# Kernel optimization log

Hardware: AMD Instinct MI355X
Metric: run time of the kernel (lower is better)

The kernel has to match this reference:

```python
import jax, jax.numpy as jnp
import numpy as np

NC = 80
REG = 16          # DFL bins per coordinate
CONF_THRES = 0.25
IOU_THRES = 0.45
MAX_DET = 300
TOPK = 1000       # fixed-size pre-NMS candidate pool (stand-in for max_nms=30000 with A=8400)
MAX_WH = 7680.0   # class offset for class-aware NMS
LEVELS = [(80, 80, 8.0), (40, 40, 16.0), (20, 20, 32.0)]  # (h, w, stride) for imgsz=640


def _make_anchors():
    """make_anchors: grid-cell centers (+0.5 offset) and per-anchor strides."""
    pts, strs = [], []
    for h, w, s in LEVELS:
        sx = jnp.arange(w, dtype=jnp.float32) + 0.5
        sy = jnp.arange(h, dtype=jnp.float32) + 0.5
        gy, gx = jnp.meshgrid(sy, sx, indexing='ij')
        pts.append(jnp.stack([gx, gy], -1).reshape(-1, 2))
        strs.append(jnp.full((h * w,), s, dtype=jnp.float32))
    return jnp.concatenate(pts).T, jnp.concatenate(strs)  # [2, A], [A]


def _box_iou(b):  # b: [K, 4] xyxy -> [K, K] pairwise IoU
    area = (b[:, 2] - b[:, 0]) * (b[:, 3] - b[:, 1])
    lt = jnp.maximum(b[:, None, :2], b[None, :, :2])
    rb = jnp.minimum(b[:, None, 2:], b[None, :, 2:])
    wh = jnp.clip(rb - lt, 0.0)
    inter = wh[..., 0] * wh[..., 1]
    return inter / (area[:, None] + area[None, :] - inter + 1e-7)


def _nms_keep(iou, valid):
    """Greedy NMS over score-sorted candidates: keep[i] iff valid and no earlier kept box overlaps > thr."""
    K = iou.shape[0]
    idx = jnp.arange(K)
    def body(keep, i):
        sup = jnp.any((iou[i] > IOU_THRES) & keep & (idx < i))
        return keep.at[i].set(valid[i] & jnp.logical_not(sup)), None
    keep, _ = jax.lax.scan(body, jnp.zeros(K, dtype=bool), idx)
    return keep


def _forward(preds, dfl_w):
    B, C, A = preds.shape
    # DFL decode: softmax over 16 bins, expectation with arange(16) weights (the 1x1 conv)
    box_logits = preds[:, :4 * REG].reshape(B, 4, REG, A)
    dist = jnp.einsum('bqra,r->bqa', jax.nn.softmax(box_logits, axis=2), dfl_w)  # [B,4,A] ltrb
    anc, strd = _make_anchors()
    lt, rb = dist[:, :2], dist[:, 2:]
    x1y1 = anc[None] - lt
    x2y2 = anc[None] + rb
    c_xy = (x1y1 + x2y2) / 2
    wh = x2y2 - x1y1
    dbox = jnp.concatenate([c_xy, wh], axis=1) * strd  # dist2bbox(xywh) * stride, [B,4,A]
    cls = jax.nn.sigmoid(preds[:, 4 * REG:])           # [B,NC,A]
    # xywh2xyxy
    cx, cy, w, h = dbox[:, 0], dbox[:, 1], dbox[:, 2], dbox[:, 3]
    boxes = jnp.stack([cx - w / 2, cy - h / 2, cx + w / 2, cy + h / 2], axis=-1)  # [B,A,4]
    conf = jnp.max(cls, axis=1)      # [B,A]
    j = jnp.argmax(cls, axis=1)      # [B,A]
    score = jnp.where(conf > CONF_THRES, conf, -1.0)
    top_s, top_i = jax.lax.top_k(score, TOPK)                               # [B,K]
    tb = jnp.take_along_axis(boxes, top_i[..., None], axis=1)               # [B,K,4]
    tj = jnp.take_along_axis(j, top_i, axis=1)                              # [B,K]
    valid = top_s > CONF_THRES
    ob = tb + (tj.astype(preds.dtype) * MAX_WH)[..., None]                  # class-offset boxes
    iou = jax.vmap(_box_iou)(ob)                                            # [B,K,K]
    keep = jax.vmap(_nms_keep)(iou, valid)                                  # [B,K]
    sel = jnp.where(keep, top_s, -1e9)
    order = jnp.argsort(-sel, axis=1)[:, :MAX_DET]                          # kept, score-sorted
    fb = jnp.take_along_axis(tb, order[..., None], axis=1)
    fs = jnp.take_along_axis(top_s, order, axis=1)
    fj = jnp.take_along_axis(tj, order, axis=1).astype(preds.dtype)
    fv = jnp.take_along_axis(keep, order, axis=1)
    out = jnp.concatenate([fb, fs[..., None], fj[..., None]], axis=-1)
    return out * fv[..., None].astype(preds.dtype)                          # [B,300,6]


def setup_inputs() -> dict:
    key = jax.random.key(0)
    k1, _ = jax.random.split(key)
    preds = jax.random.normal(k1, (32, 4 * REG + NC, 8400), dtype=jnp.float32)
    dfl_w = jnp.arange(REG, dtype=jnp.float32)
    return {"preds": preds, "dfl_w": dfl_w}


def reference(preds, dfl_w):
    return _forward(preds, dfl_w)
```

## Files before the change

kernel.cpp:

```cpp
#include <hip/hip_runtime.h>
#include <cstdint>
#include <cstddef>

typedef unsigned long long u64;
typedef unsigned int u32;

#define A_TOT   8400
#define NCLS    80
#define KSLOT   1024
#define NCHUNK  9
#define TOPK_N  1000
#define MAXDET  300
#define OUT_STRIDE (MAXDET * 6)


__device__ __forceinline__ float sig32(float x) {
#pragma clang fp contract(off)
    float e = (float)exp(-(double)x);
    float t = 1.0f + e;
    return 1.0f / t;
}

__device__ __forceinline__ u32 key_hi_from_score(float s) {
    u32 u = __float_as_uint(s);
    return (u & 0x80000000u) ? ~u : (u | 0x80000000u);
}
__device__ __forceinline__ float score_from_key_hi(u32 t) {
    u32 u = (t & 0x80000000u) ? (t ^ 0x80000000u) : ~t;
    return __uint_as_float(u);
}

__global__ void k_decode(const float* __restrict__ preds, u64* __restrict__ key_raw,
                         float4* __restrict__ dbox) {
#pragma clang fp contract(off)
    int a = blockIdx.x * blockDim.x + threadIdx.x;
    int b = blockIdx.y;
    if (a >= A_TOT) return;
    const float* pc = preds + ((size_t)b * 144 + 64) * A_TOT + a;
    const float* pd = preds + (size_t)b * 144 * A_TOT + a;

    float m = -3.0e38f, m2 = -3.0e38f;
    int jm = 0;
#pragma unroll 4
    for (int c = 0; c < NCLS; ++c) {
        float v = pc[(size_t)c * A_TOT];
        if (v > m) { m2 = m; m = v; jm = c; }
        else if (v > m2) { m2 = v; }
    }

    float conf;
    int cls = jm;
    if ((m - m2) < 1e-4f || m > 7.0f) {
        float sb = -1.0f; int jb = 0;
        for (int c = 0; c < NCLS; ++c) {
            float s = sig32(pc[(size_t)c * A_TOT]);
            if (s > sb) { sb = s; jb = c; }
        }
        conf = sb; cls = jb;
    } else {
        conf = sig32(m);
    }

    float score = (conf > 0.25f) ? conf : -1.0f;
    u32 hi = key_hi_from_score(score);
    u32 lo = ((0x3FFFu - (u32)a) << 7) | (u32)cls;
    key_raw[(size_t)b * A_TOT + a] = ((u64)hi << 32) | lo;

    int row, col; float stride;
    if (a < 6400)      { row = a / 80;          col = a % 80;          stride = 8.0f; }
    else if (a < 8000) { int aa = a - 6400; row = aa / 40; col = aa % 40; stride = 16.0f; }
    else               { int aa = a - 8000; row = aa / 20; col = aa % 20; stride = 32.0f; }
    float ax = (float)col + 0.5f;
    float ay = (float)row + 0.5f;

    float d[4];
#pragma unroll
    for (int q = 0; q < 4; ++q) {
        float x[16];
#pragma unroll
        for (int r = 0; r < 16; ++r) x[r] = pd[(size_t)(q*16 + r) * A_TOT];
        float mx = x[0];
#pragma unroll
        for (int r = 1; r < 16; ++r) mx = fmaxf(mx, x[r]);
        float e[16], s = 0.f;
#pragma unroll
        for (int r = 0; r < 16; ++r) { e[r] = expf(x[r] - mx); s = s + e[r]; }
        float dd = 0.f;
#pragma unroll
        for (int r = 0; r < 16; ++r) { float pr = e[r] / s; dd = dd + pr * (float)r; }
        d[q] = dd;
    }
    float x1 = ax - d[0], y1 = ay - d[1];
    float x2 = ax + d[2], y2 = ay + d[3];
    float cx = (x1 + x2) / 2.0f, cy = (y1 + y2) / 2.0f;
    float w  = x2 - x1,          h  = y2 - y1;
    float4 db;
    db.x = cx * stride; db.y = cy * stride; db.z = w * stride; db.w = h * stride;
    dbox[(size_t)b * A_TOT + a] = db;
}

__global__ __launch_bounds__(1024) void k_chunksort(const u64* __restrict__ key_raw,
                                                    u64* __restrict__ key_sorted) {
    __shared__ u64 s[KSLOT];
    int b = blockIdx.y, ch = blockIdx.x, t = threadIdx.x;
    int a = ch * KSLOT + t;
    s[t] = (a < A_TOT) ? key_raw[(size_t)b * A_TOT + a] : 0ull;
    __syncthreads();
    for (int k = 2; k <= KSLOT; k <<= 1) {
        for (int j = k >> 1; j > 0; j >>= 1) {
            int ixj = t ^ j;
            if (ixj > t) {
                u64 x = s[t], y = s[ixj];
                bool descBlock = ((t & k) == 0);
                bool sw = descBlock ? (x < y) : (x > y);
                if (sw) { s[t] = y; s[ixj] = x; }
            }
            __syncthreads();
        }
    }
    key_sorted[((size_t)b * NCHUNK + ch) * KSLOT + t] = s[t];
}

__global__ __launch_bounds__(1024) void k_merge(const u64* __restrict__ key_sorted,
                                                u64* __restrict__ topk) {
    __shared__ u64 R[KSLOT];
    __shared__ u64 C[KSLOT];
    int b = blockIdx.x, t = threadIdx.x;
    R[t] = key_sorted[((size_t)b * NCHUNK) * KSLOT + t];
    for (int ch = 1; ch < NCHUNK; ++ch) {
        C[t] = key_sorted[((size_t)b * NCHUNK + ch) * KSLOT + t];
        __syncthreads();
        u64 r = R[t];
        u64 c = C[(KSLOT - 1) - t];
        u64 nv = (r > c) ? r : c;
        __syncthreads();
        R[t] = nv;
        __syncthreads();
        for (int j = KSLOT >> 1; j >= 1; j >>= 1) {
            int ixj = t ^ j;
            if (ixj > t) {
                u64 x = R[t], y = R[ixj];
                if (x < y) { R[t] = y; R[ixj] = x; }
            }
            __syncthreads();
        }
    }
    topk[(size_t)b * KSLOT + t] = R[t];
}

__global__ void k_prep(const float4* __restrict__ dbox, const u64* __restrict__ topk,
                       float* __restrict__ tb, float* __restrict__ ob,
                       float* __restrict__ area, u32* __restrict__ validf) {
#pragma clang fp contract(off)
    int slot = blockIdx.x * blockDim.x + threadIdx.x;
    int b = blockIdx.y;
    if (slot >= KSLOT) return;
    size_t si = (size_t)b * KSLOT + slot;
    u64 key = topk[si];
    u32 hi = (u32)(key >> 32);
    u32 lo = (u32)key;
    bool valid = (slot < TOPK_N) && (hi & 0x80000000u);
    if (!valid) {
        tb[si*4+0]=0.f; tb[si*4+1]=0.f; tb[si*4+2]=0.f; tb[si*4+3]=0.f;
        ob[si*4+0]=0.f; ob[si*4+1]=0.f; ob[si*4+2]=0.f; ob[si*4+3]=0.f;
        area[si] = 0.f; validf[si] = 0u;
        return;
    }
    int a   = 0x3FFF - (int)((lo >> 7) & 0x3FFFu);
    int cls = (int)(lo & 0x7Fu);

    float4 db = dbox[(size_t)b * A_TOT + a];
    float bx1 = db.x - db.z / 2.0f, by1 = db.y - db.w / 2.0f;
    float bx2 = db.x + db.z / 2.0f, by2 = db.y + db.w / 2.0f;
    tb[si*4+0] = bx1; tb[si*4+1] = by1; tb[si*4+2] = bx2; tb[si*4+3] = by2;

    float off = (float)cls * 7680.0f;
    float o0 = bx1 + off, o1 = by1 + off, o2 = bx2 + off, o3 = by2 + off;
    ob[si*4+0] = o0; ob[si*4+1] = o1; ob[si*4+2] = o2; ob[si*4+3] = o3;
    area[si] = (o2 - o0) * (o3 - o1);
    validf[si] = 1u;
}

__global__ __launch_bounds__(256) void k_matrix(const float* __restrict__ ob,
                                                const float* __restrict__ area,
                                                u64* __restrict__ masks) {
#pragma clang fp contract(off)
    __shared__ float4 sob[KSLOT];
    __shared__ float  sar[KSLOT];
    int b = blockIdx.y, rblk = blockIdx.x, tid = threadIdx.x;
    const float4* gob = (const float4*)(ob + (size_t)b * KSLOT * 4);
    const float*  gar = area + (size_t)b * KSLOT;
    for (int i = tid; i < KSLOT; i += blockDim.x) { sob[i] = gob[i]; sar[i] = gar[i]; }
    __syncthreads();

    int lane = tid & 63;
    int wave = tid >> 6;
    int i = rblk * 64 + lane;
    float4 bi = sob[i];
    float Ai = sar[i];

#pragma unroll
    for (int wl = 0; wl < 4; ++wl) {
        int w = wave * 4 + wl;
        u64 mword = 0ull;
        if (w >= rblk) {
            for (int bit = 0; bit < 64; ++bit) {
                int j = (w << 6) + bit;
                float4 bj = sob[j];
                float Aj = sar[j];
                float lt0 = fmaxf(bi.x, bj.x);
                float lt1 = fmaxf(bi.y, bj.y);
                float rb0 = fminf(bi.z, bj.z);
                float rb1 = fminf(bi.w, bj.w);
                float ww = fmaxf(rb0 - lt0, 0.0f);
                float hh = fmaxf(rb1 - lt1, 0.0f);
                float inter = ww * hh;
                float den = ((Ai + Aj) - inter) + 1e-7f;
                float iou = inter / den;
                if ((j > i) && (iou > 0.45f)) mword |= (1ull << bit);
            }
        }
        masks[((size_t)b * KSLOT + i) * 16 + w] = mword;
    }
}

__global__ __launch_bounds__(64) void k_scan(const u64* __restrict__ masks,
                                             const u32* __restrict__ validf,
                                             u64* __restrict__ keep) {
    __shared__ u64 rows[KSLOT];
    int b = blockIdx.x, lane = threadIdx.x;
    const char* base = (const char*)(masks + (size_t)b * KSLOT * 16);

    float4 r0, r1, r2, r3, r4, r5, r6, r7;
    {
        const float4* src = (const float4*)base;
        r0 = src[0*64 + lane]; r1 = src[1*64 + lane];
        r2 = src[2*64 + lane]; r3 = src[3*64 + lane];
        r4 = src[4*64 + lane]; r5 = src[5*64 + lane];
        r6 = src[6*64 + lane]; r7 = src[7*64 + lane];
    }

    u64 kw = 0ull;
    u64 rem = 0ull;
    int kept = 0;

    for (int w = 0; w < 16; ++w) {
        {
            float4* dst = (float4*)rows;
            dst[0*64 + lane] = r0; dst[1*64 + lane] = r1;
            dst[2*64 + lane] = r2; dst[3*64 + lane] = r3;
            dst[4*64 + lane] = r4; dst[5*64 + lane] = r5;
            dst[6*64 + lane] = r6; dst[7*64 + lane] = r7;
        }
        u32 vf = validf[(size_t)b * KSLOT + w * 64 + lane];
        u64 valid_w = __ballot(vf != 0u);
        __syncthreads();
        if (w < 15) {
            const float4* src = (const float4*)(base + (size_t)(w + 1) * 8192);
            r0 = src[0*64 + lane]; r1 = src[1*64 + lane];
            r2 = src[2*64 + lane]; r3 = src[3*64 + lane];
            r4 = src[4*64 + lane]; r5 = src[5*64 + lane];
            r6 = src[6*64 + lane]; r7 = src[7*64 + lane];
        }

        u64 live = valid_w & ~__shfl(rem, w);
        while (live) {
            int i = __ffsll(live) - 1;
            if (lane == w) kw |= (1ull << i);
            u64 m = (lane < 16) ? rows[i * 16 + lane] : 0ull;
            rem |= m;
            ++kept;
            if (kept >= MAXDET) break;
            live &= ~(__shfl(m, w) | (1ull << i));
        }
        if (kept >= MAXDET) break;
        __syncthreads();
    }
    if (lane < 16) keep[(size_t)b * 16 + lane] = kw;
}

__global__ __launch_bounds__(1024) void k_final(const u64* __restrict__ keep,
                                                const u64* __restrict__ topk,
                                                const float* __restrict__ tb,
                                                float* __restrict__ out) {
    __shared__ u64 kw[16];
    __shared__ int pref[16];
    int b = blockIdx.x, t = threadIdx.x;
    float* ob_ = out + (size_t)b * OUT_STRIDE;
    for (int i = t; i < OUT_STRIDE; i += blockDim.x) ob_[i] = 0.0f;
    if (t < 16) kw[t] = keep[(size_t)b * 16 + t];
    __syncthreads();
    if (t == 0) {
        int s = 0;
        for (int w = 0; w < 16; ++w) { pref[w] = s; s += __popcll(kw[w]); }
    }
    __syncthreads();
    int w = t >> 6, bit = t & 63;
    bool kp = (kw[w] >> bit) & 1ull;
    if (kp) {
        u64 below = (bit == 0) ? 0ull : (kw[w] & ((1ull << bit) - 1ull));
        int rank = pref[w] + __popcll(below);
        if (rank < MAXDET) {
            size_t si = (size_t)b * KSLOT + t;
            u64 key = topk[si];
            u32 hi = (u32)(key >> 32);
            u32 lo = (u32)key;
            float score = score_from_key_hi(hi);
            float clsf = (float)(lo & 0x7Fu);
            float* o = ob_ + rank * 6;
            o[0] = tb[si*4+0]; o[1] = tb[si*4+1];
            o[2] = tb[si*4+2]; o[3] = tb[si*4+3];
            o[4] = score; o[5] = clsf;
        }
    }
}

extern "C" void kernel_launch(void* const* d_in, const int* in_sizes, int n_in,
                              void* d_out, int out_size, void* d_ws, size_t ws_size,
                              hipStream_t stream) {
    const float* preds = (const float*)d_in[0];
    float* out = (float*)d_out;
    int B = in_sizes[0] / (144 * A_TOT);

    char* ws = (char*)d_ws;
    size_t off = 0;
    u64* key_raw    = (u64*)(ws + off); off += (size_t)B * A_TOT * 8;
    u64* key_sorted = (u64*)(ws + off); off += (size_t)B * NCHUNK * KSLOT * 8;
    u64* topk       = (u64*)(ws + off); off += (size_t)B * KSLOT * 8;
    float4* dbox    = (float4*)(ws + off); off += (size_t)B * A_TOT * 16;
    float* tb       = (float*)(ws + off); off += (size_t)B * KSLOT * 4 * 4;
    float* obuf     = (float*)(ws + off); off += (size_t)B * KSLOT * 4 * 4;
    float* area     = (float*)(ws + off); off += (size_t)B * KSLOT * 4;
    u32* validf     = (u32*)(ws + off); off += (size_t)B * KSLOT * 4;
    u64* masks      = (u64*)(ws + off); off += (size_t)B * KSLOT * 16 * 8;
    u64* keep       = (u64*)(ws + off); off += (size_t)B * 16 * 8;

    k_decode<<<dim3((A_TOT + 255) / 256, B), 256, 0, stream>>>(preds, key_raw, dbox);
    k_chunksort<<<dim3(NCHUNK, B), KSLOT, 0, stream>>>(key_raw, key_sorted);
    k_merge<<<B, KSLOT, 0, stream>>>(key_sorted, topk);
    k_prep<<<dim3(KSLOT / 256, B), 256, 0, stream>>>(dbox, topk, tb, obuf, area, validf);
    k_matrix<<<dim3(16, B), 256, 0, stream>>>(obuf, area, masks);
    k_scan<<<B, 64, 0, stream>>>(masks, validf, keep);
    k_final<<<B, 1024, 0, stream>>>(keep, topk, tb, out);
}
```

Measured before the change: 200.1 us.

## Stage decode input through double-buffered LDS tiles with float4 global loads

```diff
diff --git a/kernel.cpp b/kernel.cpp
--- a/kernel.cpp
+++ b/kernel.cpp
@@ -30,26 +30,86 @@
     return __uint_as_float(u);
 }
 
-__global__ void k_decode(const float* __restrict__ preds, u64* __restrict__ key_raw,
-                         float4* __restrict__ dbox) {
+__global__ __launch_bounds__(256) void k_decode(const float* __restrict__ preds,
+                                                u64* __restrict__ key_raw,
+                                                float4* __restrict__ dbox) {
 #pragma clang fp contract(off)
-    int a = blockIdx.x * blockDim.x + threadIdx.x;
+    __shared__ float tile[2][16][256];
     int b = blockIdx.y;
-    if (a >= A_TOT) return;
-    const float* pc = preds + ((size_t)b * 144 + 64) * A_TOT + a;
-    const float* pd = preds + (size_t)b * 144 * A_TOT + a;
-
+    int a0 = blockIdx.x * 256;
+    int t = threadIdx.x;
+    int a = a0 + t;
+    int nA = A_TOT - a0; if (nA > 256) nA = 256;
+    int p4max = nA >> 2;
+    const float* pb = preds + (size_t)b * 144 * A_TOT;
+
+    int sr[4], sp[4];
+#pragma unroll
+    for (int k = 0; k < 4; ++k) { int f = t + 256 * k; sr[k] = f >> 6; sp[k] = f & 63; }
+
+    float4 regs[4];
+    auto gload = [&](int ch0) {
+#pragma unroll
+        for (int k = 0; k < 4; ++k) {
+            if (sp[k] < p4max)
+                regs[k] = *(const float4*)(pb + (size_t)(ch0 + sr[k]) * A_TOT + a0 + 4 * sp[k]);
+            else
+                regs[k] = make_float4(0.f, 0.f, 0.f, 0.f);
+        }
+    };
+    auto dswrite = [&](int buf) {
+#pragma unroll
+        for (int k = 0; k < 4; ++k)
+            *(float4*)&tile[buf][sr[k]][4 * sp[k]] = regs[k];
+    };
+
+    float d[4] = {0.f, 0.f, 0.f, 0.f};
     float m = -3.0e38f, m2 = -3.0e38f;
     int jm = 0;
-#pragma unroll 4
-    for (int c = 0; c < NCLS; ++c) {
-        float v = pc[(size_t)c * A_TOT];
-        if (v > m) { m2 = m; m = v; jm = c; }
-        else if (v > m2) { m2 = v; }
-    }
-
-    float conf;
-    int cls = jm;
+
+    gload(0); dswrite(0); __syncthreads();
+    gload(16);
+
+    for (int cb = 0; cb < 9; ++cb) {
+        int buf = cb & 1;
+        if (t < nA) {
+            float x[16];
+#pragma unroll
+            for (int r = 0; r < 16; ++r) x[r] = tile[buf][r][t];
+            if (cb < 4) {
+                float mx = x[0];
+#pragma unroll
+                for (int r = 1; r < 16; ++r) mx = fmaxf(mx, x[r]);
+                float e[16], s = 0.f;
+#pragma unroll
+                for (int r = 0; r < 16; ++r) { e[r] = expf(x[r] - mx); s = s + e[r]; }
+                float dd = 0.f;
+#pragma unroll
+                for (int r = 0; r < 16; ++r) { float pr = e[r] / s; dd = dd + pr * (float)r; }
+                d[cb] = dd;
+            } else {
+                int cbase = (cb - 4) * 16;
+#pragma unroll
+                for (int r = 0; r < 16; ++r) {
+                    int c = cbase + r;
+                    float v = x[r];
+                    if (v > m) { m2 = m; m = v; jm = c; }
+                    else if (v > m2) { m2 = v; }
+                }
+            }
+        }
+        if (cb + 1 < 9) {
+            __syncthreads();
+            dswrite((cb + 1) & 1);
+            if (cb + 2 < 9) gload((cb + 2) * 16);
+            __syncthreads();
+        }
+    }
+
+    if (t >= nA) return;
+
+    const float* pc = pb + (size_t)64 * A_TOT + a;
+    float conf; int cls = jm;
     if ((m - m2) < 1e-4f || m > 7.0f) {
         float sb = -1.0f; int jb = 0;
         for (int c = 0; c < NCLS; ++c) {
@@ -60,7 +120,6 @@
     } else {
         conf = sig32(m);
     }
-
     float score = (conf > 0.25f) ? conf : -1.0f;
     u32 hi = key_hi_from_score(score);
     u32 lo = ((0x3FFFu - (u32)a) << 7) | (u32)cls;
@@ -72,24 +131,6 @@
     else               { int aa = a - 8000; row = aa / 20; col = aa % 20; stride = 32.0f; }
     float ax = (float)col + 0.5f;
     float ay = (float)row + 0.5f;
-
-    float d[4];
-#pragma unroll
-    for (int q = 0; q < 4; ++q) {
-        float x[16];
-#pragma unroll
-        for (int r = 0; r < 16; ++r) x[r] = pd[(size_t)(q*16 + r) * A_TOT];
-        float mx = x[0];
-#pragma unroll
-        for (int r = 1; r < 16; ++r) mx = fmaxf(mx, x[r]);
-        float e[16], s = 0.f;
-#pragma unroll
-        for (int r = 0; r < 16; ++r) { e[r] = expf(x[r] - mx); s = s + e[r]; }
-        float dd = 0.f;
-#pragma unroll
-        for (int r = 0; r < 16; ++r) { float pr = e[r] / s; dd = dd + pr * (float)r; }
-        d[q] = dd;
-    }
     float x1 = ax - d[0], y1 = ay - d[1];
     float x2 = ax + d[2], y2 = ay + d[3];
     float cx = (x1 + x2) / 2.0f, cy = (y1 + y2) / 2.0f;
```

Result: faster. 167.9 us (-16.1%).
